# Optimization experiments

Measured on AMD Instinct MI355X. Metric: run time of the kernel, lower is better.

Reference implementation:

```python
import jax, jax.numpy as jnp
import numpy as np

DIM = 1024
NUM_HEADS = 16
HEAD_DIM = DIM // NUM_HEADS
INNER_ITR = 4
INNER_LR = 1.0
SCALE_QKV = 1.0


def setup_inputs() -> dict:
    key = jax.random.key(0)
    k1, k2, k3 = jax.random.split(key, 3)
    B, N, C = 8, 1024, DIM
    x = jax.random.normal(k1, (B, N, C), dtype=jnp.float32)
    # Xavier-uniform-ish scaled dense kernels
    w_qkv = jax.random.normal(k2, (C, 3 * C), dtype=jnp.float32) * (1.0 / np.sqrt(C))
    w_proj = jax.random.normal(k3, (C, C), dtype=jnp.float32) * (1.0 / np.sqrt(C))
    b_proj = jnp.zeros((C,), dtype=jnp.float32)
    return {"x": x, "w_qkv": w_qkv, "w_proj": w_proj, "b_proj": b_proj, "training": 0}


def _mttt_base(q, k, v):
    """MTTT 'base' inner loop: per (B,H) linear model W,b trained by
    INNER_ITR full-batch GD steps on MSE reconstruction of v from k,
    then applied to q. Shapes: q,k,v are (B, H, N, d)."""
    B, H, N, d = q.shape
    W = jnp.zeros((B, H, d, d), dtype=q.dtype)
    b = jnp.zeros((B, H, 1, d), dtype=q.dtype)
    invN = 1.0 / N
    for _ in range(INNER_ITR):  # small fixed iteration count
        pred = jnp.einsum('bhnd,bhde->bhne', k, W) + b   # (B,H,N,d)
        err = pred - v
        gW = jnp.einsum('bhnd,bhne->bhde', k, err) * invN
        gb = jnp.mean(err, axis=2, keepdims=True)
        W = W - INNER_LR * gW
        b = b - INNER_LR * gb
    return jnp.einsum('bhnd,bhde->bhne', q, W) + b       # (B,H,N,d)


def reference(x, w_qkv, w_proj, b_proj, training):
    B, N, C = x.shape
    H, d = NUM_HEADS, HEAD_DIM
    qkv = jnp.einsum('bnc,ce->bne', x, w_qkv)            # (B,N,3C), qkv_bias=False
    qkv = qkv.reshape(B, N, 3, H, d).transpose(2, 0, 3, 1, 4)  # (3,B,H,N,d)
    qkv = qkv * SCALE_QKV
    q, k, v = qkv[0], qkv[1], qkv[2]
    # qk_norm=False -> identity; scale_q=False -> no q scaling
    out = _mttt_base(q, k, v)                            # (B,H,N,d)
    out = out.transpose(0, 2, 1, 3).reshape(B, N, C)
    out = jnp.einsum('bnc,cd->bnd', out, w_proj) + b_proj
    # proj dropout deterministic (training=False)
    return out
```

## Files before the change

### kernel.cpp

```cpp
#include <hip/hip_runtime.h>


#define SEQ    1024
#define NBATCH 8
#define DIMC   1024
#define NHEAD  16
#define HDIM   64
#define MROWS  8192
#define NQKV   3072

typedef __attribute__((ext_vector_type(8))) __bf16 bf16x8;
typedef __attribute__((ext_vector_type(4))) float  f32x4;

__device__ __forceinline__ unsigned short f2b(float f) {
  union { float f; unsigned int u; } v; v.f = f;
  unsigned int r = (v.u + 0x7FFFu + ((v.u >> 16) & 1u)) >> 16;
  return (unsigned short)r;
}
__device__ __forceinline__ float b2f(unsigned short u) {
  union { unsigned int u; float f; } v; v.u = ((unsigned int)u) << 16;
  return v.f;
}

__device__ __forceinline__ void load_lds16(const void* g, void* l) {
  __builtin_amdgcn_global_load_lds(
      (__attribute__((address_space(1))) void*)(void*)(g),
      (__attribute__((address_space(3))) void*)(l), 16, 0, 0);
}

#define FENCE asm volatile("" ::: "memory")
#define BAR   __builtin_amdgcn_s_barrier()
#define LGKM0 do { asm volatile("s_waitcnt lgkmcnt(0)" ::: "memory"); \
                   __builtin_amdgcn_sched_barrier(0); } while (0)
#define PRIO1 __builtin_amdgcn_s_setprio(1)
#define PRIO0 __builtin_amdgcn_s_setprio(0)

#define WAITVM(n_) do {                                                    \
    if ((n_) == 0) asm volatile("s_waitcnt vmcnt(0)" ::: "memory");        \
    else if ((n_) == 4) asm volatile("s_waitcnt vmcnt(4)" ::: "memory");   \
    else if ((n_) == 6) asm volatile("s_waitcnt vmcnt(6)" ::: "memory");   \
    else asm volatile("s_waitcnt vmcnt(8)" ::: "memory");                  \
  } while (0)

__global__ __launch_bounds__(256) void cvt_bf16(const float* __restrict__ in,
                                                unsigned short* __restrict__ out,
                                                int n4) {
  int i = blockIdx.x * 256 + threadIdx.x;
  if (i >= n4) return;
  float4 v = ((const float4*)in)[i];
  ushort4 o;
  o.x = f2b(v.x); o.y = f2b(v.y); o.z = f2b(v.z); o.w = f2b(v.w);
  ((ushort4*)out)[i] = o;
}

__global__ __launch_bounds__(256) void transpose_cvt(const float* __restrict__ in,
                                                     unsigned short* __restrict__ out,
                                                     int R, int Cc) {
  __shared__ unsigned short tile[32][33];
  int c0 = blockIdx.x * 32, r0 = blockIdx.y * 32;
  int tx = threadIdx.x, ty = threadIdx.y;
  for (int i = ty; i < 32; i += 8)
    tile[i][tx] = f2b(in[(size_t)(r0 + i) * Cc + c0 + tx]);
  __syncthreads();
  for (int i = ty; i < 32; i += 8)
    out[(size_t)(c0 + i) * R + r0 + tx] = tile[tx][i];
}

template <int BM, int STORE_F32>
__global__ __launch_bounds__(512, 2) void gemm_p8(const unsigned short* __restrict__ A,
                                                  const unsigned short* __restrict__ BT,
                                                  void* __restrict__ Cout,
                                                  const float* __restrict__ bias,
                                                  int N, int NBN) {
  constexpr int MI = BM / 32;
  constexpr int MH = MI / 2;
  constexpr int ABYTES = BM * 128;
  constexpr int BBYTES = 32768;
  constexpr int BUFB = ABYTES + BBYTES;
  constexpr int ACALLS = BM / 128;
  constexpr int NTC = 4 + 2 * ACALLS;

  extern __shared__ __align__(16) char ldsb[];

  const int tid = threadIdx.x;
  const int lane = tid & 63, wave = tid >> 6;
  const int wr = wave >> 2, wc = wave & 3;
  const int frow = lane & 15;
  const int g4 = lane >> 4;
  const int cz0 = (g4 ^ (lane & 7)) * 16;
  const int cz1 = ((4 | g4) ^ (lane & 7)) * 16;

  const int cpx = gridDim.x >> 3;
  const int wg = (blockIdx.x & 7) * cpx + (blockIdx.x >> 3);
  const int bm = wg / NBN, bn = wg % NBN;
  const size_t m0 = (size_t)bm * BM, n0 = (size_t)bn * 256;

  const int srow = tid >> 3;
  const int scol = ((tid & 7) ^ ((tid >> 3) & 7)) * 8;
  const unsigned short* srcA = A + (m0 + srow) * 1024 + scol;
  const unsigned short* srcB = BT + (n0 + srow) * 1024 + scol;

  const int aBase = (wr * (BM / 2) + frow) * 128;
  const int bBase = (wc * 64 + frow) * 128;

  f32x4 acc[MI][4];
  if (STORE_F32) {
#pragma unroll
    for (int j = 0; j < 4; ++j) {
      float4 bv = *(const float4*)&bias[n0 + wc * 64 + j * 16 + g4 * 4];
      f32x4 t; t[0] = bv.x; t[1] = bv.y; t[2] = bv.z; t[3] = bv.w;
#pragma unroll
      for (int i = 0; i < MI; ++i) acc[i][j] = t;
    }
  } else {
#pragma unroll
    for (int i = 0; i < MI; ++i)
#pragma unroll
      for (int j = 0; j < 4; ++j) acc[i][j] = f32x4{0.f, 0.f, 0.f, 0.f};
  }

  auto stageA = [&](int buf_, int h_, int tt_) {
    char* dst = ldsb + buf_ * BUFB + h_ * (ABYTES / 2) + wave * 1024;
    const unsigned short* s = srcA + (size_t)(h_ * (BM / 2)) * 1024 + tt_ * 64;
    load_lds16(s, dst);
    if constexpr (ACALLS == 2) load_lds16(s + 65536, dst + 8192);
  };
  auto stageB = [&](int buf_, int h_, int tt_) {
    char* dst = ldsb + buf_ * BUFB + ABYTES + h_ * 16384 + wave * 1024;
    const unsigned short* s = srcB + (size_t)(h_ * 128) * 1024 + tt_ * 64;
    load_lds16(s, dst);
    load_lds16(s + 65536, dst + 8192);
  };

#define READ_A(buf_, mh_, dst_) do {                                     \
    const char* ab_ = ldsb + (buf_) * BUFB + aBase + (mh_) * (MH * 2048);\
    _Pragma("unroll") for (int fi = 0; fi < MH; ++fi) {                  \
      dst_[fi][0] = *(const bf16x8*)(ab_ + fi * 2048 + cz0);             \
      dst_[fi][1] = *(const bf16x8*)(ab_ + fi * 2048 + cz1); }           \
  } while (0)

#define READ_B(buf_, nh_, dst_) do {                                     \
    const char* bb_ = ldsb + (buf_) * BUFB + ABYTES + bBase + (nh_) * 4096;\
    _Pragma("unroll") for (int fj = 0; fj < 2; ++fj) {                   \
      dst_[fj][0] = *(const bf16x8*)(bb_ + fj * 2048 + cz0);             \
      dst_[fj][1] = *(const bf16x8*)(bb_ + fj * 2048 + cz1); }           \
  } while (0)

#define MFMAQ(mh_, nh_, bb_)                                             \
    _Pragma("unroll") for (int fi = 0; fi < MH; ++fi)                    \
    _Pragma("unroll") for (int fj = 0; fj < 2; ++fj)                     \
    _Pragma("unroll") for (int kk = 0; kk < 2; ++kk)                     \
      acc[(mh_) * MH + fi][(nh_) * 2 + fj] =                             \
        __builtin_amdgcn_mfma_f32_16x16x32_bf16(bb_[fj][kk], aq[fi][kk], \
            acc[(mh_) * MH + fi][(nh_) * 2 + fj], 0, 0, 0)

  stageB(0, 0, 0); stageB(0, 1, 0); stageA(0, 0, 0); stageA(0, 1, 0);
  stageB(1, 0, 1); stageB(1, 1, 1); stageA(1, 0, 1); stageA(1, 1, 1);
  WAITVM(NTC);
  FENCE; BAR;

#pragma unroll 1
  for (int it = 0; it < 8; ++it) {
    const int st = (it < 7);
    const int t2 = 2 * it + 2, t3 = 2 * it + 3;
    bf16x8 aq[MH][2], b0[2][2], b1[2][2];
    READ_A(0, 0, aq); READ_B(0, 0, b0);
    FENCE; BAR; LGKM0;
    PRIO1; MFMAQ(0, 0, b0); PRIO0; FENCE; BAR;
    READ_B(0, 1, b1);
    FENCE; BAR; LGKM0;
    PRIO1; MFMAQ(0, 1, b1); PRIO0; FENCE; BAR;
    READ_A(0, 1, aq);
    if (st) stageB(0, 0, t2);
    FENCE; BAR; LGKM0;
    PRIO1; MFMAQ(1, 0, b0); PRIO0; FENCE; BAR;
    if (st) stageB(0, 1, t2);
    FENCE; BAR; LGKM0;
    PRIO1; MFMAQ(1, 1, b1); PRIO0;
    if (st) WAITVM(4); else WAITVM(0);
    FENCE; BAR;
    READ_A(1, 0, aq); READ_B(1, 0, b0);
    if (st) stageA(0, 0, t2);
    FENCE; BAR; LGKM0;
    PRIO1; MFMAQ(0, 0, b0); PRIO0; FENCE; BAR;
    READ_B(1, 1, b1);
    if (st) stageA(0, 1, t2);
    FENCE; BAR; LGKM0;
    PRIO1; MFMAQ(0, 1, b1); PRIO0; FENCE; BAR;
    READ_A(1, 1, aq);
    if (st) stageB(1, 0, t3);
    FENCE; BAR; LGKM0;
    PRIO1; MFMAQ(1, 0, b0); PRIO0; FENCE; BAR;
    if (st) { stageB(1, 1, t3); stageA(1, 0, t3); stageA(1, 1, t3); }
    FENCE; BAR; LGKM0;
    PRIO1; MFMAQ(1, 1, b1); PRIO0;
    WAITVM(NTC);
    FENCE; BAR;
  }
#undef READ_A
#undef READ_B
#undef MFMAQ

  const size_t mbase = m0 + wr * (BM / 2) + frow;
  const size_t nbase = n0 + wc * 64 + g4 * 4;
  if (STORE_F32) {
    float* C = (float*)Cout;
#pragma unroll
    for (int i = 0; i < MI; ++i)
#pragma unroll
      for (int j = 0; j < 4; ++j) {
        float4 o; o.x = acc[i][j][0]; o.y = acc[i][j][1];
        o.z = acc[i][j][2]; o.w = acc[i][j][3];
        *(float4*)&C[(mbase + i * 16) * N + nbase + j * 16] = o;
      }
  } else {
    unsigned short* C = (unsigned short*)Cout;
#pragma unroll
    for (int i = 0; i < MI; ++i)
#pragma unroll
      for (int j = 0; j < 4; ++j) {
        ushort4 o; o.x = f2b(acc[i][j][0]); o.y = f2b(acc[i][j][1]);
        o.z = f2b(acc[i][j][2]); o.w = f2b(acc[i][j][3]);
        *(ushort4*)&C[(mbase + i * 16) * N + nbase + j * 16] = o;
      }
  }
}

__global__ __launch_bounds__(256) void transpose_kv(const unsigned short* __restrict__ qkvb,
                                                    unsigned short* __restrict__ kt,
                                                    unsigned short* __restrict__ vt) {
  __shared__ unsigned short tile[64][80];
  const int nc = blockIdx.x * 64;
  const int bh = blockIdx.y;
  const int which = blockIdx.z;
  const int b = bh >> 4, h = bh & 15;
  const int tid = threadIdx.x;
  const unsigned short* src = qkvb + (size_t)(b * SEQ + nc) * NQKV + (which + 1) * DIMC + h * HDIM;
  for (int idx = tid; idx < 512; idx += 256) {
    int rr = idx >> 3, ss = (idx & 7) * 8;
    *(uint4*)&tile[rr][ss] = *(const uint4*)&src[(size_t)rr * NQKV + ss];
  }
  __syncthreads();
  unsigned short* dst = (which ? vt : kt) + (size_t)bh * HDIM * SEQ;
  for (int idx = tid; idx < 512; idx += 256) {
    int dd = idx >> 3, ns = (idx & 7) * 8;
    alignas(16) unsigned short tmp[8];
#pragma unroll
    for (int jj = 0; jj < 8; ++jj) tmp[jj] = tile[ns + jj][dd];
    *(uint4*)&dst[(size_t)dd * SEQ + nc + ns] = *(const uint4*)tmp;
  }
}

__global__ __launch_bounds__(256) void stats_gd(const unsigned short* __restrict__ kt,
                                                const unsigned short* __restrict__ vt,
                                                unsigned short* __restrict__ Wtb,
                                                float* __restrict__ bvec) {
  __shared__ float Gs[64][68];
  __shared__ float Ps[64][68];
  __shared__ float Ws[64][68];
  __shared__ float mkp[4][64], mvp[4][64];
  __shared__ float mks[64], mvs[64], bs[64];

  const int bh = blockIdx.x;
  const int tid = threadIdx.x;
  const int lane = tid & 63, wave = tid >> 6;
  const unsigned short* kb = kt + (size_t)bh * HDIM * SEQ;
  const unsigned short* vb = vt + (size_t)bh * HDIM * SEQ;
  const int frow = lane & 15;
  const int fk = (lane >> 4) * 8;

  f32x4 accG[4], accP[4];
#pragma unroll
  for (int j = 0; j < 4; ++j) {
    accG[j] = f32x4{0.f, 0.f, 0.f, 0.f};
    accP[j] = f32x4{0.f, 0.f, 0.f, 0.f};
  }
  for (int nb = 0; nb < SEQ; nb += 32) {
    bf16x8 af = *(const bf16x8*)&kb[(size_t)(wave * 16 + frow) * SEQ + nb + fk];
    bf16x8 kf[4], vf[4];
#pragma unroll
    for (int j = 0; j < 4; ++j)
      kf[j] = *(const bf16x8*)&kb[(size_t)(j * 16 + frow) * SEQ + nb + fk];
#pragma unroll
    for (int j = 0; j < 4; ++j)
      vf[j] = *(const bf16x8*)&vb[(size_t)(j * 16 + frow) * SEQ + nb + fk];
#pragma unroll
    for (int j = 0; j < 4; ++j) {
      accG[j] = __builtin_amdgcn_mfma_f32_16x16x32_bf16(af, kf[j], accG[j], 0, 0, 0);
      accP[j] = __builtin_amdgcn_mfma_f32_16x16x32_bf16(af, vf[j], accP[j], 0, 0, 0);
    }
  }
  const float invN = 1.0f / (float)SEQ;
  const int orow = wave * 16 + (lane >> 4) * 4;
#pragma unroll
  for (int j = 0; j < 4; ++j)
#pragma unroll
    for (int r = 0; r < 4; ++r) {
      Gs[orow + r][j * 16 + frow] = accG[j][r] * invN;
      Ps[orow + r][j * 16 + frow] = accP[j][r] * invN;
    }

  {
    float sk_ = 0.f, sv_ = 0.f;
    const unsigned short* kr = &kb[(size_t)lane * SEQ + wave * 256];
    const unsigned short* vr = &vb[(size_t)lane * SEQ + wave * 256];
    for (int nn = 0; nn < 256; nn += 8) {
      uint4 a = *(const uint4*)&kr[nn];
      uint4 c = *(const uint4*)&vr[nn];
      const unsigned short* pa = (const unsigned short*)&a;
      const unsigned short* pc = (const unsigned short*)&c;
#pragma unroll
      for (int jj = 0; jj < 8; ++jj) { sk_ += b2f(pa[jj]); sv_ += b2f(pc[jj]); }
    }
    mkp[wave][lane] = sk_;
    mvp[wave][lane] = sv_;
  }
  __syncthreads();

  const int r = tid >> 2;
  const int c0 = (tid & 3) * 16;
  if (tid < 64) {
    mks[tid] = (mkp[0][tid] + mkp[1][tid] + mkp[2][tid] + mkp[3][tid]) * invN;
    mvs[tid] = (mvp[0][tid] + mvp[1][tid] + mvp[2][tid] + mvp[3][tid]) * invN;
    bs[tid] = 0.f;
  }
#pragma unroll
  for (int c = 0; c < 16; ++c) Ws[r][c0 + c] = 0.f;
  __syncthreads();

  for (int it = 0; it < 4; ++it) {
    float wn[16];
#pragma unroll
    for (int c = 0; c < 16; ++c)
      wn[c] = Ws[r][c0 + c] + Ps[r][c0 + c] - mks[r] * bs[c0 + c];
    for (int j = 0; j < 64; ++j) {
      float g = Gs[r][j];
#pragma unroll
      for (int c = 0; c < 16; ++c) wn[c] -= g * Ws[j][c0 + c];
    }
    float bn = 0.f;
    if (tid < 64) {
      bn = mvs[tid];
      for (int j = 0; j < 64; ++j) bn -= mks[j] * Ws[j][tid];
    }
    __syncthreads();
#pragma unroll
    for (int c = 0; c < 16; ++c) Ws[r][c0 + c] = wn[c];
    if (tid < 64) bs[tid] = bn;
    __syncthreads();
  }

  unsigned short* wout = Wtb + (size_t)bh * HDIM * HDIM;
#pragma unroll
  for (int c = 0; c < 16; ++c)
    wout[(size_t)(c0 + c) * HDIM + r] = f2b(Ws[r][c0 + c]);
  if (tid < 64) bvec[(size_t)bh * HDIM + tid] = bs[tid];
}

__global__ __launch_bounds__(256) void attn_qw(const unsigned short* __restrict__ qkvb,
                                               const unsigned short* __restrict__ Wtb,
                                               const float* __restrict__ bvec,
                                               unsigned short* __restrict__ attnb) {
  const int h = blockIdx.y;
  const int m0 = blockIdx.x * 128;
  const int bh = ((m0 >> 10) << 4) + h;
  const int tid = threadIdx.x;
  const int lane = tid & 63, wave = tid >> 6;
  const int frow = lane & 15;
  const int fk = (lane >> 4) * 8;

  f32x4 acc[2][4];
#pragma unroll
  for (int j = 0; j < 4; ++j) {
    float bv = bvec[(size_t)bh * HDIM + j * 16 + frow];
    f32x4 t; t[0] = bv; t[1] = bv; t[2] = bv; t[3] = bv;
    acc[0][j] = t; acc[1][j] = t;
  }

  const unsigned short* qbase = qkvb + (size_t)(m0 + wave * 32) * NQKV + h * HDIM;
  const unsigned short* wbase = Wtb + (size_t)bh * HDIM * HDIM;
#pragma unroll
  for (int s = 0; s < 2; ++s) {
    bf16x8 af[2], wf[4];
#pragma unroll
    for (int i = 0; i < 2; ++i)
      af[i] = *(const bf16x8*)&qbase[(size_t)(i * 16 + frow) * NQKV + s * 32 + fk];
#pragma unroll
    for (int j = 0; j < 4; ++j)
      wf[j] = *(const bf16x8*)&wbase[(size_t)(j * 16 + frow) * HDIM + s * 32 + fk];
#pragma unroll
    for (int i = 0; i < 2; ++i)
#pragma unroll
      for (int j = 0; j < 4; ++j)
        acc[i][j] = __builtin_amdgcn_mfma_f32_16x16x32_bf16(af[i], wf[j], acc[i][j], 0, 0, 0);
  }

  const int orow = m0 + wave * 32 + (lane >> 4) * 4;
#pragma unroll
  for (int i = 0; i < 2; ++i)
#pragma unroll
    for (int j = 0; j < 4; ++j)
#pragma unroll
      for (int rr = 0; rr < 4; ++rr)
        attnb[(size_t)(orow + i * 16 + rr) * DIMC + h * HDIM + j * 16 + frow] = f2b(acc[i][j][rr]);
}

extern "C" void kernel_launch(void* const* d_in, const int* in_sizes, int n_in,
                              void* d_out, int out_size, void* d_ws, size_t ws_size,
                              hipStream_t stream) {
  const float* x      = (const float*)d_in[0];
  const float* w_qkv  = (const float*)d_in[1];
  const float* w_proj = (const float*)d_in[2];
  const float* b_proj = (const float*)d_in[3];

  char* ws = (char*)d_ws;
  unsigned short* xb    = (unsigned short*)(ws + 0);
  unsigned short* wqT   = (unsigned short*)(ws + 16777216);
  unsigned short* wpT   = (unsigned short*)(ws + 23068672);
  unsigned short* qkvb  = (unsigned short*)(ws + 25165824);
  unsigned short* kt    = (unsigned short*)(ws + 75497472);
  unsigned short* vt    = (unsigned short*)(ws + 92274688);
  unsigned short* attnb = (unsigned short*)(ws + 109051904);
  unsigned short* Wtb   = (unsigned short*)(ws + 125829120);
  float*          bvec  = (float*)(ws + 126877696);
  if (ws_size < (size_t)126910464) return;

  hipFuncSetAttribute((const void*)gemm_p8<256, 0>,
                      hipFuncAttributeMaxDynamicSharedMemorySize, 131072);
  hipFuncSetAttribute((const void*)gemm_p8<128, 1>,
                      hipFuncAttributeMaxDynamicSharedMemorySize, 131072);

  cvt_bf16<<<8192, 256, 0, stream>>>(x, xb, MROWS * DIMC / 4);
  transpose_cvt<<<dim3(96, 32), dim3(32, 8), 0, stream>>>(w_qkv, wqT, 1024, 3072);
  transpose_cvt<<<dim3(32, 32), dim3(32, 8), 0, stream>>>(w_proj, wpT, 1024, 1024);
  gemm_p8<256, 0><<<dim3(384), dim3(512), 131072, stream>>>(xb, wqT, qkvb, nullptr, NQKV, 12);
  transpose_kv<<<dim3(16, 128, 2), 256, 0, stream>>>(qkvb, kt, vt);
  stats_gd<<<128, 256, 0, stream>>>(kt, vt, Wtb, bvec);
  attn_qw<<<dim3(64, 16), 256, 0, stream>>>(qkvb, Wtb, bvec, attnb);
  gemm_p8<128, 1><<<dim3(256), dim3(512), 98304, stream>>>(attnb, wpT, d_out, b_proj, DIMC, 4);
}
```

Measured before the change: 198.0 us.

## Software-pipeline LDS fragment reads and global stages across MFMA quadrants in GEMM

Restructures the GEMM main loop so LDS fragment reads for the next quadrant are issued before the current quadrant's MFMAs. It uses double-buffered A register fragments (aX/aY) and drops the per-quadrant lgkmcnt(0) waits. Global-to-LDS stage loads are spread more evenly, with a finer vmcnt wait after each quadrant. The aim is to hide LDS and global latency behind MFMA work. The cost is higher register pressure and finer-grained wait-count correctness that depends on BM.

```diff
diff --git a/kernel.cpp b/kernel.cpp
--- a/kernel.cpp
+++ b/kernel.cpp
@@ -28,19 +28,11 @@
       (__attribute__((address_space(3))) void*)(l), 16, 0, 0);
 }
 
-#define FENCE asm volatile("" ::: "memory")
-#define BAR   __builtin_amdgcn_s_barrier()
-#define LGKM0 do { asm volatile("s_waitcnt lgkmcnt(0)" ::: "memory"); \
-                   __builtin_amdgcn_sched_barrier(0); } while (0)
-#define PRIO1 __builtin_amdgcn_s_setprio(1)
-#define PRIO0 __builtin_amdgcn_s_setprio(0)
-
-#define WAITVM(n_) do {                                                    \
-    if ((n_) == 0) asm volatile("s_waitcnt vmcnt(0)" ::: "memory");        \
-    else if ((n_) == 4) asm volatile("s_waitcnt vmcnt(4)" ::: "memory");   \
-    else if ((n_) == 6) asm volatile("s_waitcnt vmcnt(6)" ::: "memory");   \
-    else asm volatile("s_waitcnt vmcnt(8)" ::: "memory");                  \
-  } while (0)
+#define FENCE  asm volatile("" ::: "memory")
+#define BAR    __builtin_amdgcn_s_barrier()
+#define PRIO1  __builtin_amdgcn_s_setprio(1)
+#define PRIO0  __builtin_amdgcn_s_setprio(0)
+#define SCHED0 __builtin_amdgcn_sched_barrier(0)
 
 __global__ __launch_bounds__(256) void cvt_bf16(const float* __restrict__ in,
                                                 unsigned short* __restrict__ out,
@@ -75,10 +67,8 @@
   constexpr int MI = BM / 32;
   constexpr int MH = MI / 2;
   constexpr int ABYTES = BM * 128;
-  constexpr int BBYTES = 32768;
-  constexpr int BUFB = ABYTES + BBYTES;
+  constexpr int BUFB = ABYTES + 32768;
   constexpr int ACALLS = BM / 128;
-  constexpr int NTC = 4 + 2 * ACALLS;
 
   extern __shared__ __align__(16) char ldsb[];
 
@@ -146,60 +136,76 @@
       dst_[fj][1] = *(const bf16x8*)(bb_ + fj * 2048 + cz1); }           \
   } while (0)
 
-#define MFMAQ(mh_, nh_, bb_)                                             \
+#define MFMAQ(mh_, nh_, as_, bs_)                                        \
     _Pragma("unroll") for (int fi = 0; fi < MH; ++fi)                    \
     _Pragma("unroll") for (int fj = 0; fj < 2; ++fj)                     \
     _Pragma("unroll") for (int kk = 0; kk < 2; ++kk)                     \
       acc[(mh_) * MH + fi][(nh_) * 2 + fj] =                             \
-        __builtin_amdgcn_mfma_f32_16x16x32_bf16(bb_[fj][kk], aq[fi][kk], \
+        __builtin_amdgcn_mfma_f32_16x16x32_bf16(bs_[fj][kk], as_[fi][kk],\
             acc[(mh_) * MH + fi][(nh_) * 2 + fj], 0, 0, 0)
 
-  stageB(0, 0, 0); stageB(0, 1, 0); stageA(0, 0, 0); stageA(0, 1, 0);
-  stageB(1, 0, 1); stageB(1, 1, 1); stageA(1, 0, 1); stageA(1, 1, 1);
-  WAITVM(NTC);
+#define VMW(st_) do {                                                    \
+    if (st_) {                                                           \
+      if constexpr (BM == 256)                                           \
+        asm volatile("s_waitcnt vmcnt(4)" ::: "memory");                 \
+      else                                                               \
+        asm volatile("s_waitcnt vmcnt(3)" ::: "memory");                 \
+    } else {                                                             \
+      asm volatile("s_waitcnt vmcnt(0)" ::: "memory");                   \
+    }                                                                    \
+  } while (0)
+
+  bf16x8 aX[MH][2], aY[MH][2], b0[2][2], b1[2][2];
+
+  stageB(0, 0, 0); stageA(0, 0, 0); stageA(0, 1, 0); stageB(0, 1, 0);
+  stageB(1, 0, 1); stageA(1, 0, 1); stageA(1, 1, 1);
+  if constexpr (BM == 256) asm volatile("s_waitcnt vmcnt(6)" ::: "memory");
+  else                     asm volatile("s_waitcnt vmcnt(4)" ::: "memory");
+  FENCE; BAR;
+  READ_A(0, 0, aX); READ_B(0, 0, b0);
+  asm volatile("s_waitcnt lgkmcnt(0)" ::: "memory");
+  SCHED0;
   FENCE; BAR;
 
 #pragma unroll 1
   for (int it = 0; it < 8; ++it) {
     const int st = (it < 7);
-    const int t2 = 2 * it + 2, t3 = 2 * it + 3;
-    bf16x8 aq[MH][2], b0[2][2], b1[2][2];
-    READ_A(0, 0, aq); READ_B(0, 0, b0);
-    FENCE; BAR; LGKM0;
-    PRIO1; MFMAQ(0, 0, b0); PRIO0; FENCE; BAR;
+    const int t1 = 2 * it + 1, t2 = 2 * it + 2, t3 = 2 * it + 3;
     READ_B(0, 1, b1);
-    FENCE; BAR; LGKM0;
-    PRIO1; MFMAQ(0, 1, b1); PRIO0; FENCE; BAR;
-    READ_A(0, 1, aq);
+    stageB(1, 1, t1);
+    SCHED0;
+    PRIO1; MFMAQ(0, 0, aX, b0); PRIO0; VMW(st); FENCE; BAR;
+    READ_A(0, 1, aY);
     if (st) stageB(0, 0, t2);
-    FENCE; BAR; LGKM0;
-    PRIO1; MFMAQ(1, 0, b0); PRIO0; FENCE; BAR;
+    SCHED0;
+    PRIO1; MFMAQ(0, 1, aX, b1); PRIO0; VMW(st); FENCE; BAR;
+    READ_A(1, 0, aX);
+    if (st) stageA(0, 0, t2);
+    SCHED0;
+    PRIO1; MFMAQ(1, 0, aY, b0); PRIO0; VMW(st); FENCE; BAR;
+    READ_B(1, 0, b0);
+    if (st) stageA(0, 1, t2);
+    SCHED0;
+    PRIO1; MFMAQ(1, 1, aY, b1); PRIO0; VMW(st); FENCE; BAR;
+    READ_B(1, 1, b1);
     if (st) stageB(0, 1, t2);
-    FENCE; BAR; LGKM0;
-    PRIO1; MFMAQ(1, 1, b1); PRIO0;
-    if (st) WAITVM(4); else WAITVM(0);
-    FENCE; BAR;
-    READ_A(1, 0, aq); READ_B(1, 0, b0);
-    if (st) stageA(0, 0, t2);
-    FENCE; BAR; LGKM0;
-    PRIO1; MFMAQ(0, 0, b0); PRIO0; FENCE; BAR;
-    READ_B(1, 1, b1);
-    if (st) stageA(0, 1, t2);
-    FENCE; BAR; LGKM0;
-    PRIO1; MFMAQ(0, 1, b1); PRIO0; FENCE; BAR;
-    READ_A(1, 1, aq);
+    SCHED0;
+    PRIO1; MFMAQ(0, 0, aX, b0); PRIO0; VMW(st); FENCE; BAR;
+    READ_A(1, 1, aY);
     if (st) stageB(1, 0, t3);
-    FENCE; BAR; LGKM0;
-    PRIO1; MFMAQ(1, 0, b0); PRIO0; FENCE; BAR;
-    if (st) { stageB(1, 1, t3); stageA(1, 0, t3); stageA(1, 1, t3); }
-    FENCE; BAR; LGKM0;
-    PRIO1; MFMAQ(1, 1, b1); PRIO0;
-    WAITVM(NTC);
-    FENCE; BAR;
+    SCHED0;
+    PRIO1; MFMAQ(0, 1, aX, b1); PRIO0; VMW(st); FENCE; BAR;
+    if (st) { READ_A(0, 0, aX); stageA(1, 0, t3); }
+    SCHED0;
+    PRIO1; MFMAQ(1, 0, aY, b0); PRIO0; VMW(st); FENCE; BAR;
+    if (st) { READ_B(0, 0, b0); stageA(1, 1, t3); }
+    SCHED0;
+    PRIO1; MFMAQ(1, 1, aY, b1); PRIO0; VMW(st); FENCE; BAR;
   }
 #undef READ_A
 #undef READ_B
 #undef MFMAQ
+#undef VMW
 
   const size_t mbase = m0 + wr * (BM / 2) + frow;
   const size_t nbase = n0 + wc * 64 + g4 * 4;
```

Measured after the change: 195.7 us. Within noise of the previous version (-1.2%).
